# Kernel optimization log

Measured on AMD Instinct MI355X. Metric: run time of the kernel, lower is better.

The kernel has to match this reference:

```python
import jax, jax.numpy as jnp
import numpy as np

B, T, DM = 1, 8192, 1024
DS, DC, EXP = 16, 4, 2
DI = DM * EXP  # 2048


def setup_inputs() -> dict:
    key = jax.random.key(0)
    ks = jax.random.split(key, 6)
    sc = lambda k, shape, s: jax.random.normal(k, shape, jnp.float32) * s
    return {
        "x": jax.random.normal(ks[0], (B, T, DM), jnp.float32),
        "W_in": sc(ks[1], (DM, 2 * DI), 0.02),        # stored [in, out]
        "conv_w": sc(ks[2], (DI, 1, DC), 0.2),        # depthwise conv weight (OIH)
        "conv_b": jnp.zeros((DI,), jnp.float32),
        "W_x": sc(ks[3], (DI, 2 * DS + 1), 0.02),     # stored [in, out]
        "A_log": jnp.log(jnp.arange(1, DS + 1, dtype=jnp.float32)),
        "D": jnp.ones((DI,), jnp.float32),
        "W_out": sc(ks[4], (DI, DM), 0.02),           # stored [in, out]
    }


def reference(x, W_in, conv_w, conv_b, W_x, A_log, D, W_out):
    Bq, Tq, _ = x.shape
    # input projection and gate split
    xz = x @ W_in                              # [B,T,2*DI]
    xc, z = jnp.split(xz, 2, axis=-1)          # each [B,T,DI]
    # causal depthwise conv1d (pad left DC-1 == torch pad both + truncate [:T])
    xcT = jnp.transpose(xc, (0, 2, 1))         # [B,DI,T]
    conv = jax.lax.conv_general_dilated(
        xcT, conv_w, window_strides=(1,), padding=[(DC - 1, 0)],
        feature_group_count=DI)
    conv = conv + conv_b[None, :, None]
    xs = jax.nn.silu(jnp.transpose(conv, (0, 2, 1)))   # [B,T,DI]
    # selective SSM parameters (single shared delta per timestep)
    x_dbl = xs @ W_x                           # [B,T,2N+1]
    delta = jax.nn.softplus(x_dbl[..., :1])    # [B,T,1]
    Bp = x_dbl[..., 1:1 + DS]                  # [B,T,N]
    Cp = x_dbl[..., 1 + DS:]                   # [B,T,N]
    A = -jnp.exp(A_log)                        # [N]
    A_bar = jnp.exp(delta * A)                 # [B,T,N]
    B_bar = delta * Bp                         # [B,T,N]

    def step(h, inp):
        a_t, b_t, x_t, c_t = inp               # [B,N],[B,N],[B,DI],[B,N]
        h = a_t[:, None, :] * h + b_t[:, None, :] * x_t[:, :, None]  # [B,DI,N]
        y_t = jnp.einsum('bdn,bn->bd', h, c_t)
        return h, y_t

    h0 = jnp.zeros((Bq, DI, DS), xs.dtype)
    seq = (jnp.swapaxes(A_bar, 0, 1), jnp.swapaxes(B_bar, 0, 1),
           jnp.swapaxes(xs, 0, 1), jnp.swapaxes(Cp, 0, 1))
    _, ys = jax.lax.scan(step, h0, seq)        # ys: [T,B,DI]
    y = jnp.swapaxes(ys, 0, 1) + D * xs        # [B,T,DI]
    y = y * jax.nn.silu(z)
    return y @ W_out                           # [B,T,DM]
```

## Files before the change

kernel.cpp:

```cpp
#include <hip/hip_runtime.h>
#include <hip/hip_bf16.h>

#define T_SEQ 8192
#define DMODEL 1024
#define DINNER 2048
#define NSTATE 16
#define NCH 128
#define CL 64

typedef __attribute__((ext_vector_type(8))) short bf16x8;
typedef __attribute__((ext_vector_type(4))) float f32x4;

__device__ __forceinline__ float bf2f(ushort u) {
  union { unsigned u; float f; } c; c.u = ((unsigned)u) << 16; return c.f;
}
__device__ __forceinline__ ushort f2bf(float f) {
  union { float f; unsigned u; } c; c.f = f;
  unsigned r = c.u + 0x7FFFu + ((c.u >> 16) & 1u);
  return (ushort)(r >> 16);
}

#define GLD16(dst, src) __builtin_amdgcn_global_load_lds( \
    (const __attribute__((address_space(1))) void*)(src), \
    (__attribute__((address_space(3))) void*)(dst), 16, 0, 0)

template<int N> __device__ __forceinline__ void waitcnt_vm() {
  asm volatile("s_waitcnt vmcnt(%0)" :: "i"(N) : "memory");
}
#define LGKM0() do { asm volatile("s_waitcnt lgkmcnt(0)" ::: "memory"); \
                     __builtin_amdgcn_sched_barrier(0); } while (0)

__global__ __launch_bounds__(256) void cast_bf16(const float* __restrict__ in,
                                                 ushort* __restrict__ out, int n4) {
  int i = blockIdx.x * 256 + threadIdx.x;
  if (i < n4) {
    float4 v = ((const float4*)in)[i];
    ushort4 o;
    o.x = f2bf(v.x); o.y = f2bf(v.y); o.z = f2bf(v.z); o.w = f2bf(v.w);
    ((ushort4*)out)[i] = o;
  }
}

__global__ __launch_bounds__(256) void transpose_bf16(const float* __restrict__ in,
                                                      ushort* __restrict__ out, int R, int C) {
  __shared__ float tile[32][33];
  int bx = blockIdx.x * 32;
  int by = blockIdx.y * 32;
  int x = threadIdx.x, y = threadIdx.y;
#pragma unroll
  for (int j = 0; j < 32; j += 8)
    tile[y + j][x] = in[(size_t)(by + y + j) * C + bx + x];
  __syncthreads();
#pragma unroll
  for (int j = 0; j < 32; j += 8)
    out[(size_t)(bx + y + j) * R + by + x] = f2bf(tile[x][y + j]);
}

__global__ __launch_bounds__(256) void wx_transpose_pad(const float* __restrict__ Wx,
                                                        ushort* __restrict__ wxT) {
  int idx = blockIdx.x * 256 + threadIdx.x;
  int j = idx >> 11;
  int k = idx & 2047;
  wxT[idx] = (j < 33) ? f2bf(Wx[k * 33 + j]) : (ushort)0;
}

template<int OUTMODE>
__global__ __launch_bounds__(512, 2)
void gemm_pipe(const ushort* __restrict__ A, const ushort* __restrict__ B,
               void* __restrict__ out0, void* __restrict__ out1,
               int N, int K, int nbn) {
  extern __shared__ __align__(16) char smem[];
  char* const smemB = smem + 98304;

  const int tid = threadIdx.x, lane = tid & 63, wid = tid >> 6;
  const int wm = wid >> 1, wn = wid & 1;

  const int nwg = gridDim.x;
  const int q = nwg >> 3, r = nwg & 7;
  const int xcd = blockIdx.x & 7, bidx = blockIdx.x >> 3;
  const int wg = (xcd < r ? xcd * (q + 1) : r * (q + 1) + (xcd - r) * q) + bidx;
  const int mbase = (wg / nbn) * 256;
  const int nbase = (wg % nbn) * 128;
  const int NT = K >> 6;

  const int srow = tid >> 3;
  const int scb = ((tid & 7) << 4) ^ ((srow & 7) << 4);
  const ushort* pa[4];
  const ushort* pb[2];
#pragma unroll
  for (int j = 0; j < 4; ++j) pa[j] = A + (size_t)(mbase + j * 64 + srow) * K + (scb >> 1);
#pragma unroll
  for (int j = 0; j < 2; ++j) pb[j] = B + (size_t)(nbase + j * 64 + srow) * K + (scb >> 1);

#define STA(buf, j, tt) GLD16(smem  + (buf) * 32768 + (j) * 8192 + wid * 1024, pa[j] + (size_t)(tt) * 64)
#define STB(buf, j, tt) GLD16(smemB + (buf) * 16384 + (j) * 8192 + wid * 1024, pb[j] + (size_t)(tt) * 64)

  const int frow = lane & 15, hh = lane >> 4;
  const int cbk0 = (hh << 4) ^ ((frow & 7) << 4);
  const int cbk1 = (64 + (hh << 4)) ^ ((frow & 7) << 4);
  const int arow0 = (wm * 64 + frow) * 128;
  const int brow0 = (wn * 64 + frow) * 128;

  f32x4 acc[4][4];
#pragma unroll
  for (int m = 0; m < 4; ++m)
#pragma unroll
    for (int n = 0; n < 4; ++n) acc[m][n] = (f32x4){0.f, 0.f, 0.f, 0.f};

#pragma unroll
  for (int tt = 0; tt < 2; ++tt) {
    STA(tt, 0, tt); STA(tt, 1, tt); STA(tt, 2, tt); STA(tt, 3, tt);
    STB(tt, 0, tt); STB(tt, 1, tt);
  }
  waitcnt_vm<6>();
  __builtin_amdgcn_s_barrier();

  int cur = 0;
  for (int t = 0; t < NT; ++t) {
    const char* bA = smem + cur * 32768;
    const char* bB = smemB + cur * 16384;
    const int nxt = cur + 2 - ((cur >= 1) ? 3 : 0);
    const bool pf = (t + 2 < NT);
    bf16x8 alo[2][2], ahi[2][2], blo[2][2], bhi[2][2];

#pragma unroll
    for (int m = 0; m < 2; ++m) {
      alo[m][0] = *(const bf16x8*)(bA + arow0 + m * 2048 + cbk0);
      alo[m][1] = *(const bf16x8*)(bA + arow0 + m * 2048 + cbk1);
    }
#pragma unroll
    for (int n = 0; n < 2; ++n) {
      blo[n][0] = *(const bf16x8*)(bB + brow0 + n * 2048 + cbk0);
      blo[n][1] = *(const bf16x8*)(bB + brow0 + n * 2048 + cbk1);
    }
    if (pf) { STA(nxt, 0, t + 2); STA(nxt, 1, t + 2); }
    __builtin_amdgcn_s_barrier();
    LGKM0();
    __builtin_amdgcn_s_setprio(1);
#pragma unroll
    for (int m = 0; m < 2; ++m)
#pragma unroll
      for (int n = 0; n < 2; ++n)
#pragma unroll
        for (int kk = 0; kk < 2; ++kk)
          acc[m][n] = __builtin_amdgcn_mfma_f32_16x16x32_bf16(alo[m][kk], blo[n][kk], acc[m][n], 0, 0, 0);
    __builtin_amdgcn_s_setprio(0);
    __builtin_amdgcn_s_barrier();

#pragma unroll
    for (int m = 0; m < 2; ++m) {
      ahi[m][0] = *(const bf16x8*)(bA + arow0 + (2 + m) * 2048 + cbk0);
      ahi[m][1] = *(const bf16x8*)(bA + arow0 + (2 + m) * 2048 + cbk1);
    }
    if (pf) { STA(nxt, 2, t + 2); STA(nxt, 3, t + 2); }
    __builtin_amdgcn_s_barrier();
    LGKM0();
    __builtin_amdgcn_s_setprio(1);
#pragma unroll
    for (int m = 0; m < 2; ++m)
#pragma unroll
      for (int n = 0; n < 2; ++n)
#pragma unroll
        for (int kk = 0; kk < 2; ++kk)
          acc[2 + m][n] = __builtin_amdgcn_mfma_f32_16x16x32_bf16(ahi[m][kk], blo[n][kk], acc[2 + m][n], 0, 0, 0);
    __builtin_amdgcn_s_setprio(0);
    __builtin_amdgcn_s_barrier();

#pragma unroll
    for (int n = 0; n < 2; ++n) {
      bhi[n][0] = *(const bf16x8*)(bB + brow0 + (2 + n) * 2048 + cbk0);
      bhi[n][1] = *(const bf16x8*)(bB + brow0 + (2 + n) * 2048 + cbk1);
    }
    if (pf) STB(nxt, 0, t + 2);
    __builtin_amdgcn_s_barrier();
    LGKM0();
    __builtin_amdgcn_s_setprio(1);
#pragma unroll
    for (int m = 0; m < 2; ++m)
#pragma unroll
      for (int n = 0; n < 2; ++n)
#pragma unroll
        for (int kk = 0; kk < 2; ++kk)
          acc[2 + m][2 + n] = __builtin_amdgcn_mfma_f32_16x16x32_bf16(ahi[m][kk], bhi[n][kk], acc[2 + m][2 + n], 0, 0, 0);
    __builtin_amdgcn_s_setprio(0);
    __builtin_amdgcn_s_barrier();

    if (pf) STB(nxt, 1, t + 2);
    __builtin_amdgcn_s_setprio(1);
#pragma unroll
    for (int m = 0; m < 2; ++m)
#pragma unroll
      for (int n = 0; n < 2; ++n)
#pragma unroll
        for (int kk = 0; kk < 2; ++kk)
          acc[m][2 + n] = __builtin_amdgcn_mfma_f32_16x16x32_bf16(alo[m][kk], bhi[n][kk], acc[m][2 + n], 0, 0, 0);
    __builtin_amdgcn_s_setprio(0);
    if (pf) waitcnt_vm<6>(); else waitcnt_vm<0>();
    __builtin_amdgcn_s_barrier();

    cur = cur + 1 - ((cur == 2) ? 3 : 0);
  }

  const int crow0 = mbase + wm * 64 + (lane >> 4) * 4;
  const int ccol0 = nbase + wn * 64 + (lane & 15);
#pragma unroll
  for (int m = 0; m < 4; ++m)
#pragma unroll
    for (int n = 0; n < 4; ++n)
#pragma unroll
      for (int j = 0; j < 4; ++j) {
        int rr = crow0 + m * 16 + j;
        int cc = ccol0 + n * 16;
        float v = acc[m][n][j];
        if (OUTMODE == 0) {
          ((float*)out0)[(size_t)rr * N + cc] = v;
        } else {
          ushort* dst = (cc < 2048) ? (ushort*)out0 : (ushort*)out1;
          int c2 = cc & 2047;
          dst[(size_t)rr * 2048 + c2] = f2bf(v);
        }
      }
#undef STA
#undef STB
}

__global__ __launch_bounds__(256) void gemm_thin(const ushort* __restrict__ A,
                                                 const ushort* __restrict__ Bw,
                                                 float* __restrict__ part) {
  __shared__ __align__(16) ushort sA[128 * 64];
  __shared__ __align__(16) ushort sB[48 * 64];
  const int tid = threadIdx.x, lane = tid & 63, wid = tid >> 6;
  const int mbase = blockIdx.x * 128;
  const int kbase = blockIdx.y * 512;
  const int frow = lane & 15, fke = (lane >> 4) * 8;

  f32x4 acc[2][3];
#pragma unroll
  for (int m = 0; m < 2; ++m)
#pragma unroll
    for (int n = 0; n < 3; ++n) acc[m][n] = (f32x4){0.f, 0.f, 0.f, 0.f};

  for (int k0 = 0; k0 < 512; k0 += 64) {
#pragma unroll
    for (int j = 0; j < 4; ++j) {
      int o = tid * 16 + j * 4096;
      int row = o >> 7, ke = ((o >> 4) & 7) * 8;
      GLD16((char*)sA + wid * 1024 + j * 4096,
            A + (size_t)(mbase + row) * DINNER + kbase + k0 + ke);
    }
    for (int i = tid; i < 384; i += 256) {
      int brow = i >> 3, kc = (i & 7) * 8;
      *(bf16x8*)&sB[brow * 64 + kc] = *(const bf16x8*)(Bw + (size_t)brow * DINNER + kbase + k0 + kc);
    }
    __syncthreads();
    bf16x8 af[2][2], bf_[3][2];
#pragma unroll
    for (int m = 0; m < 2; ++m)
#pragma unroll
      for (int ks = 0; ks < 2; ++ks)
        af[m][ks] = *(const bf16x8*)&sA[(wid * 32 + m * 16 + frow) * 64 + ks * 32 + fke];
#pragma unroll
    for (int n = 0; n < 3; ++n)
#pragma unroll
      for (int ks = 0; ks < 2; ++ks)
        bf_[n][ks] = *(const bf16x8*)&sB[(n * 16 + frow) * 64 + ks * 32 + fke];
#pragma unroll
    for (int m = 0; m < 2; ++m)
#pragma unroll
      for (int n = 0; n < 3; ++n)
#pragma unroll
        for (int ks = 0; ks < 2; ++ks)
          acc[m][n] = __builtin_amdgcn_mfma_f32_16x16x32_bf16(af[m][ks], bf_[n][ks], acc[m][n], 0, 0, 0);
    __syncthreads();
  }
  float* po = part + (size_t)blockIdx.y * (T_SEQ * 48);
#pragma unroll
  for (int m = 0; m < 2; ++m)
#pragma unroll
    for (int n = 0; n < 3; ++n)
#pragma unroll
      for (int j = 0; j < 4; ++j) {
        int rr = mbase + wid * 32 + m * 16 + (lane >> 4) * 4 + j;
        int cc = n * 16 + (lane & 15);
        po[(size_t)rr * 48 + cc] = acc[m][n][j];
      }
}

__global__ __launch_bounds__(256) void reduce4(const float* __restrict__ part,
                                               float* __restrict__ xdbl) {
  int i = blockIdx.x * 256 + threadIdx.x;
  const float4* p = (const float4*)part;
  float4 a = p[i], b = p[i + 98304], c = p[i + 2 * 98304], d = p[i + 3 * 98304];
  ((float4*)xdbl)[i] = make_float4(a.x + b.x + c.x + d.x, a.y + b.y + c.y + d.y,
                                   a.z + b.z + c.z + d.z, a.w + b.w + c.w + d.w);
}

__global__ __launch_bounds__(256) void conv_silu(const ushort* __restrict__ xc,
                                                 const float* __restrict__ cw,
                                                 const float* __restrict__ cb,
                                                 ushort* __restrict__ xs) {
  int idx = blockIdx.x * 256 + threadIdx.x;
  int t = idx >> 11, d = idx & 2047;
  float4 w = *(const float4*)(cw + d * 4);
  float a = cb[d];
  const float wk[4] = {w.x, w.y, w.z, w.w};
#pragma unroll
  for (int k = 0; k < 4; ++k) {
    int tt = t - 3 + k;
    if (tt >= 0) a += bf2f(xc[(size_t)tt * 2048 + d]) * wk[k];
  }
  float s = a / (1.f + expf(-a));
  xs[idx] = f2bf(s);
}

__global__ __launch_bounds__(256) void precompute_k(const float* __restrict__ xdbl,
                                                    const float* __restrict__ A_log,
                                                    float* __restrict__ abar,
                                                    float* __restrict__ bbar,
                                                    float* __restrict__ cc,
                                                    float* __restrict__ dlt) {
  int t = blockIdx.x * 256 + threadIdx.x;
  if (t >= T_SEQ) return;
  const float* r = xdbl + (size_t)t * 48;
  float v = r[0];
  float delta = (v > 20.f) ? v : log1pf(expf(v));
  dlt[t] = delta;
#pragma unroll
  for (int n = 0; n < NSTATE; ++n) {
    float A = -expf(A_log[n]);
    abar[t * 16 + n] = expf(delta * A);
    bbar[t * 16 + n] = delta * r[1 + n];
    cc[t * 16 + n]   = r[17 + n];
  }
}

__global__ __launch_bounds__(256) void chunkprod_k(const float* __restrict__ dlt,
                                                   const float* __restrict__ A_log,
                                                   float* __restrict__ P) {
  int idx = blockIdx.x * 256 + threadIdx.x;
  if (idx >= NCH * NSTATE) return;
  int c = idx >> 4, n = idx & 15;
  float s = 0.f;
  for (int i = 0; i < CL; ++i) s += dlt[c * CL + i];
  P[idx] = expf(-expf(A_log[n]) * s);
}

__global__ __launch_bounds__(256) void scan1(const ushort* __restrict__ xs,
                                             const float* __restrict__ abar,
                                             const float* __restrict__ bbar,
                                             float* __restrict__ hend) {
  int c = blockIdx.x;
  int d = blockIdx.y * 256 + threadIdx.x;
  __shared__ float s_ab[CL * 16], s_bb[CL * 16];
  for (int e = threadIdx.x; e < CL * 16; e += 256) {
    s_ab[e] = abar[(size_t)c * CL * 16 + e];
    s_bb[e] = bbar[(size_t)c * CL * 16 + e];
  }
  __syncthreads();
  float h[16];
#pragma unroll
  for (int n = 0; n < 16; ++n) h[n] = 0.f;
  int tbase = c * CL;
  for (int i = 0; i < CL; ++i) {
    float x = bf2f(xs[(size_t)(tbase + i) * DINNER + d]);
#pragma unroll
    for (int n = 0; n < 16; ++n) h[n] = s_ab[i * 16 + n] * h[n] + s_bb[i * 16 + n] * x;
  }
  float* o = hend + ((size_t)c * DINNER + d) * 16;
#pragma unroll
  for (int qq = 0; qq < 4; ++qq)
    ((float4*)o)[qq] = make_float4(h[4 * qq], h[4 * qq + 1], h[4 * qq + 2], h[4 * qq + 3]);
}

__global__ __launch_bounds__(256) void scan2(const float* __restrict__ hend,
                                             const float* __restrict__ P,
                                             float* __restrict__ hin) {
  int idx = blockIdx.x * 256 + threadIdx.x;
  int n = idx & 15;
  float h = 0.f;
  for (int c = 0; c < NCH; ++c) {
    hin[(size_t)c * (DINNER * 16) + idx] = h;
    h = P[c * 16 + n] * h + hend[(size_t)c * (DINNER * 16) + idx];
  }
}

__global__ __launch_bounds__(256) void scan3(const ushort* __restrict__ xs,
                                             const ushort* __restrict__ zb,
                                             const float* __restrict__ abar,
                                             const float* __restrict__ bbar,
                                             const float* __restrict__ cc,
                                             const float* __restrict__ hin,
                                             const float* __restrict__ Dv,
                                             ushort* __restrict__ y) {
  int c = blockIdx.x;
  int d = blockIdx.y * 256 + threadIdx.x;
  __shared__ float s_ab[CL * 16], s_bb[CL * 16], s_cc[CL * 16];
  for (int e = threadIdx.x; e < CL * 16; e += 256) {
    s_ab[e] = abar[(size_t)c * CL * 16 + e];
    s_bb[e] = bbar[(size_t)c * CL * 16 + e];
    s_cc[e] = cc[(size_t)c * CL * 16 + e];
  }
  __syncthreads();
  float h[16];
  const float* hi = hin + ((size_t)c * DINNER + d) * 16;
#pragma unroll
  for (int qq = 0; qq < 4; ++qq) {
    float4 v = ((const float4*)hi)[qq];
    h[4 * qq] = v.x; h[4 * qq + 1] = v.y; h[4 * qq + 2] = v.z; h[4 * qq + 3] = v.w;
  }
  float Dd = Dv[d];
  int tbase = c * CL;
  for (int i = 0; i < CL; ++i) {
    size_t t = tbase + i;
    float x = bf2f(xs[t * DINNER + d]);
    float ys = 0.f;
#pragma unroll
    for (int n = 0; n < 16; ++n) {
      h[n] = s_ab[i * 16 + n] * h[n] + s_bb[i * 16 + n] * x;
      ys += s_cc[i * 16 + n] * h[n];
    }
    float z = bf2f(zb[t * 2048 + d]);
    float yv = (ys + Dd * x) * (z / (1.f + expf(-z)));
    y[t * DINNER + d] = f2bf(yv);
  }
}

extern "C" void kernel_launch(void* const* d_in, const int* in_sizes, int n_in,
                              void* d_out, int out_size, void* d_ws, size_t ws_size,
                              hipStream_t stream) {
  const float* x      = (const float*)d_in[0];
  const float* W_in   = (const float*)d_in[1];
  const float* conv_w = (const float*)d_in[2];
  const float* conv_b = (const float*)d_in[3];
  const float* W_x    = (const float*)d_in[4];
  const float* A_log  = (const float*)d_in[5];
  const float* Dv     = (const float*)d_in[6];
  const float* W_out  = (const float*)d_in[7];
  float* out = (float*)d_out;

  char* w = (char*)d_ws;
  auto alloc = [&](size_t bytes) { char* p = w; w += (bytes + 255) & ~(size_t)255; return p; };

  ushort* xbf   = (ushort*)alloc((size_t)T_SEQ * DMODEL * 2);
  ushort* winT  = (ushort*)alloc((size_t)4096 * 1024 * 2);
  ushort* woutT = (ushort*)alloc((size_t)1024 * 2048 * 2);
  ushort* wxT   = (ushort*)alloc((size_t)48 * 2048 * 2);
  ushort* xc    = (ushort*)alloc((size_t)T_SEQ * DINNER * 2);
  ushort* zb    = (ushort*)alloc((size_t)T_SEQ * DINNER * 2);
  ushort* xs    = (ushort*)alloc((size_t)T_SEQ * DINNER * 2);
  float*  xdbl  = (float*) alloc((size_t)T_SEQ * 48 * 4);
  float*  parts = (float*) alloc((size_t)4 * T_SEQ * 48 * 4);
  float*  abar  = (float*) alloc((size_t)T_SEQ * 16 * 4);
  float*  bbar  = (float*) alloc((size_t)T_SEQ * 16 * 4);
  float*  ccb   = (float*) alloc((size_t)T_SEQ * 16 * 4);
  float*  dlt   = (float*) alloc((size_t)T_SEQ * 4);
  float*  P     = (float*) alloc((size_t)NCH * 16 * 4);
  float*  hend  = (float*) alloc((size_t)NCH * DINNER * 16 * 4);
  float*  hin   = (float*) alloc((size_t)NCH * DINNER * 16 * 4);
  ushort* ybf   = (ushort*)alloc((size_t)T_SEQ * DINNER * 2);

  auto kg1 = gemm_pipe<1>;
  auto kg3 = gemm_pipe<0>;
  hipFuncSetAttribute(reinterpret_cast<const void*>(kg1),
                      hipFuncAttributeMaxDynamicSharedMemorySize, 147456);
  hipFuncSetAttribute(reinterpret_cast<const void*>(kg3),
                      hipFuncAttributeMaxDynamicSharedMemorySize, 147456);

  cast_bf16<<<(T_SEQ * DMODEL / 4 + 255) / 256, 256, 0, stream>>>(x, xbf, T_SEQ * DMODEL / 4);
  transpose_bf16<<<dim3(4096 / 32, 1024 / 32), dim3(32, 8), 0, stream>>>(W_in, winT, 1024, 4096);
  transpose_bf16<<<dim3(1024 / 32, 2048 / 32), dim3(32, 8), 0, stream>>>(W_out, woutT, 2048, 1024);
  wx_transpose_pad<<<(48 * 2048) / 256, 256, 0, stream>>>(W_x, wxT);

  kg1<<<dim3((T_SEQ / 256) * (4096 / 128)), 512, 147456, stream>>>(xbf, winT, xc, zb, 4096, 1024, 4096 / 128);

  conv_silu<<<(T_SEQ * DINNER) / 256, 256, 0, stream>>>(xc, conv_w, conv_b, xs);

  gemm_thin<<<dim3(T_SEQ / 128, 4), 256, 0, stream>>>(xs, wxT, parts);
  reduce4<<<(T_SEQ * 48 / 4) / 256, 256, 0, stream>>>(parts, xdbl);

  precompute_k<<<T_SEQ / 256, 256, 0, stream>>>(xdbl, A_log, abar, bbar, ccb, dlt);
  chunkprod_k<<<(NCH * 16 + 255) / 256, 256, 0, stream>>>(dlt, A_log, P);

  scan1<<<dim3(NCH, DINNER / 256), 256, 0, stream>>>(xs, abar, bbar, hend);
  scan2<<<(DINNER * 16) / 256, 256, 0, stream>>>(hend, P, hin);
  scan3<<<dim3(NCH, DINNER / 256), 256, 0, stream>>>(xs, zb, abar, bbar, ccb, hin, Dv, ybf);

  kg3<<<dim3((T_SEQ / 256) * (1024 / 128)), 512, 147456, stream>>>(ybf, woutT, out, nullptr, 1024, 2048, 1024 / 128);
}
```

Baseline: 316.8 us.

## Restructure GEMM to 128x256 tiles with 4 waves and K=32 steps; vectorize conv

New measurement: 375.1 us. 18.4% more time.

```diff
diff --git a/kernel.cpp b/kernel.cpp
--- a/kernel.cpp
+++ b/kernel.cpp
@@ -29,6 +29,8 @@
 }
 #define LGKM0() do { asm volatile("s_waitcnt lgkmcnt(0)" ::: "memory"); \
                      __builtin_amdgcn_sched_barrier(0); } while (0)
+#define BAR() do { __builtin_amdgcn_sched_barrier(0); __builtin_amdgcn_s_barrier(); \
+                   __builtin_amdgcn_sched_barrier(0); } while (0)
 
 __global__ __launch_bounds__(256) void cast_bf16(const float* __restrict__ in,
                                                  ushort* __restrict__ out, int n4) {
@@ -65,163 +67,132 @@
 }
 
 template<int OUTMODE>
-__global__ __launch_bounds__(512, 2)
+__global__ __launch_bounds__(256, 2)
 void gemm_pipe(const ushort* __restrict__ A, const ushort* __restrict__ B,
                void* __restrict__ out0, void* __restrict__ out1,
                int N, int K, int nbn) {
   extern __shared__ __align__(16) char smem[];
-  char* const smemB = smem + 98304;
+  char* const sBb = smem + 3 * 8192;
 
   const int tid = threadIdx.x, lane = tid & 63, wid = tid >> 6;
-  const int wm = wid >> 1, wn = wid & 1;
+  const int wn = wid;
 
   const int nwg = gridDim.x;
   const int q = nwg >> 3, r = nwg & 7;
   const int xcd = blockIdx.x & 7, bidx = blockIdx.x >> 3;
   const int wg = (xcd < r ? xcd * (q + 1) : r * (q + 1) + (xcd - r) * q) + bidx;
-  const int mbase = (wg / nbn) * 256;
-  const int nbase = (wg % nbn) * 128;
-  const int NT = K >> 6;
-
-  const int srow = tid >> 3;
-  const int scb = ((tid & 7) << 4) ^ ((srow & 7) << 4);
-  const ushort* pa[4];
-  const ushort* pb[2];
-#pragma unroll
-  for (int j = 0; j < 4; ++j) pa[j] = A + (size_t)(mbase + j * 64 + srow) * K + (scb >> 1);
-#pragma unroll
-  for (int j = 0; j < 2; ++j) pb[j] = B + (size_t)(nbase + j * 64 + srow) * K + (scb >> 1);
-
-#define STA(buf, j, tt) GLD16(smem  + (buf) * 32768 + (j) * 8192 + wid * 1024, pa[j] + (size_t)(tt) * 64)
-#define STB(buf, j, tt) GLD16(smemB + (buf) * 16384 + (j) * 8192 + wid * 1024, pb[j] + (size_t)(tt) * 64)
+  const int mbase = (wg / nbn) * 128;
+  const int nbase = (wg % nbn) * 256;
+  const int NT = K >> 5;
+
+  const ushort* pa[2];
+  const ushort* pb[4];
+#pragma unroll
+  for (int j = 0; j < 2; ++j) {
+    int idx = j * 256 + wid * 64 + lane;
+    int row = idx >> 2, g = idx & 3;
+    pa[j] = A + (size_t)(mbase + row) * K + (g ^ (row & 3)) * 8;
+  }
+#pragma unroll
+  for (int j = 0; j < 4; ++j) {
+    int idx = j * 256 + wid * 64 + lane;
+    int row = idx >> 2, g = idx & 3;
+    pb[j] = B + (size_t)(nbase + row) * K + (g ^ (row & 3)) * 8;
+  }
+
+#define STA(slot, tt) do { char* _d = smem + (slot) * 8192 + wid * 1024; \
+    GLD16(_d,        pa[0] + (size_t)(tt) * 32); \
+    GLD16(_d + 4096, pa[1] + (size_t)(tt) * 32); } while (0)
+#define STB01(slot, tt) do { char* _d = sBb + (slot) * 16384 + wid * 1024; \
+    GLD16(_d,        pb[0] + (size_t)(tt) * 32); \
+    GLD16(_d + 4096, pb[1] + (size_t)(tt) * 32); } while (0)
+#define STB23(slot, tt) do { char* _d = sBb + (slot) * 16384 + 8192 + wid * 1024; \
+    GLD16(_d,        pb[2] + (size_t)(tt) * 32); \
+    GLD16(_d + 4096, pb[3] + (size_t)(tt) * 32); } while (0)
 
   const int frow = lane & 15, hh = lane >> 4;
-  const int cbk0 = (hh << 4) ^ ((frow & 7) << 4);
-  const int cbk1 = (64 + (hh << 4)) ^ ((frow & 7) << 4);
-  const int arow0 = (wm * 64 + frow) * 128;
-  const int brow0 = (wn * 64 + frow) * 128;
-
-  f32x4 acc[4][4];
-#pragma unroll
-  for (int m = 0; m < 4; ++m)
+  const int gsw = (hh ^ (frow & 3)) << 4;
+  const int aoff = frow * 64 + gsw;
+  const int boff = (wn * 64 + frow) * 64 + gsw;
+
+  f32x4 acc[8][4];
+#pragma unroll
+  for (int m = 0; m < 8; ++m)
 #pragma unroll
     for (int n = 0; n < 4; ++n) acc[m][n] = (f32x4){0.f, 0.f, 0.f, 0.f};
 
-#pragma unroll
-  for (int tt = 0; tt < 2; ++tt) {
-    STA(tt, 0, tt); STA(tt, 1, tt); STA(tt, 2, tt); STA(tt, 3, tt);
-    STB(tt, 0, tt); STB(tt, 1, tt);
-  }
+  STA(0, 0); STB01(0, 0); STB23(0, 0);
+  STA(1, 1); STB01(1, 1); STB23(1, 1);
   waitcnt_vm<6>();
-  __builtin_amdgcn_s_barrier();
+  BAR();
 
   int cur = 0;
   for (int t = 0; t < NT; ++t) {
-    const char* bA = smem + cur * 32768;
-    const char* bB = smemB + cur * 16384;
+    const char* bA = smem + cur * 8192;
+    const char* bB = sBb + cur * 16384;
     const int nxt = cur + 2 - ((cur >= 1) ? 3 : 0);
     const bool pf = (t + 2 < NT);
-    bf16x8 alo[2][2], ahi[2][2], blo[2][2], bhi[2][2];
-
-#pragma unroll
-    for (int m = 0; m < 2; ++m) {
-      alo[m][0] = *(const bf16x8*)(bA + arow0 + m * 2048 + cbk0);
-      alo[m][1] = *(const bf16x8*)(bA + arow0 + m * 2048 + cbk1);
-    }
-#pragma unroll
-    for (int n = 0; n < 2; ++n) {
-      blo[n][0] = *(const bf16x8*)(bB + brow0 + n * 2048 + cbk0);
-      blo[n][1] = *(const bf16x8*)(bB + brow0 + n * 2048 + cbk1);
-    }
-    if (pf) { STA(nxt, 0, t + 2); STA(nxt, 1, t + 2); }
-    __builtin_amdgcn_s_barrier();
+    bf16x8 a[8], b0, b1, b2, b3;
+
+#pragma unroll
+    for (int m = 0; m < 8; ++m) a[m] = *(const bf16x8*)(bA + aoff + m * 1024);
+    b0 = *(const bf16x8*)(bB + boff);
+    b1 = *(const bf16x8*)(bB + boff + 1024);
+    if (pf) { STA(nxt, t + 2); STB01(nxt, t + 2); }
+    BAR();
     LGKM0();
     __builtin_amdgcn_s_setprio(1);
 #pragma unroll
-    for (int m = 0; m < 2; ++m)
-#pragma unroll
-      for (int n = 0; n < 2; ++n)
-#pragma unroll
-        for (int kk = 0; kk < 2; ++kk)
-          acc[m][n] = __builtin_amdgcn_mfma_f32_16x16x32_bf16(alo[m][kk], blo[n][kk], acc[m][n], 0, 0, 0);
+    for (int m = 0; m < 8; ++m) {
+      acc[m][0] = __builtin_amdgcn_mfma_f32_16x16x32_bf16(a[m], b0, acc[m][0], 0, 0, 0);
+      acc[m][1] = __builtin_amdgcn_mfma_f32_16x16x32_bf16(a[m], b1, acc[m][1], 0, 0, 0);
+    }
     __builtin_amdgcn_s_setprio(0);
-    __builtin_amdgcn_s_barrier();
-
-#pragma unroll
-    for (int m = 0; m < 2; ++m) {
-      ahi[m][0] = *(const bf16x8*)(bA + arow0 + (2 + m) * 2048 + cbk0);
-      ahi[m][1] = *(const bf16x8*)(bA + arow0 + (2 + m) * 2048 + cbk1);
-    }
-    if (pf) { STA(nxt, 2, t + 2); STA(nxt, 3, t + 2); }
-    __builtin_amdgcn_s_barrier();
+    BAR();
+
+    b2 = *(const bf16x8*)(bB + boff + 2048);
+    b3 = *(const bf16x8*)(bB + boff + 3072);
+    if (pf) STB23(nxt, t + 2);
+    BAR();
     LGKM0();
     __builtin_amdgcn_s_setprio(1);
 #pragma unroll
-    for (int m = 0; m < 2; ++m)
-#pragma unroll
-      for (int n = 0; n < 2; ++n)
-#pragma unroll
-        for (int kk = 0; kk < 2; ++kk)
-          acc[2 + m][n] = __builtin_amdgcn_mfma_f32_16x16x32_bf16(ahi[m][kk], blo[n][kk], acc[2 + m][n], 0, 0, 0);
-    __builtin_amdgcn_s_setprio(0);
-    __builtin_amdgcn_s_barrier();
-
-#pragma unroll
-    for (int n = 0; n < 2; ++n) {
-      bhi[n][0] = *(const bf16x8*)(bB + brow0 + (2 + n) * 2048 + cbk0);
-      bhi[n][1] = *(const bf16x8*)(bB + brow0 + (2 + n) * 2048 + cbk1);
-    }
-    if (pf) STB(nxt, 0, t + 2);
-    __builtin_amdgcn_s_barrier();
-    LGKM0();
-    __builtin_amdgcn_s_setprio(1);
-#pragma unroll
-    for (int m = 0; m < 2; ++m)
-#pragma unroll
-      for (int n = 0; n < 2; ++n)
-#pragma unroll
-        for (int kk = 0; kk < 2; ++kk)
-          acc[2 + m][2 + n] = __builtin_amdgcn_mfma_f32_16x16x32_bf16(ahi[m][kk], bhi[n][kk], acc[2 + m][2 + n], 0, 0, 0);
-    __builtin_amdgcn_s_setprio(0);
-    __builtin_amdgcn_s_barrier();
-
-    if (pf) STB(nxt, 1, t + 2);
-    __builtin_amdgcn_s_setprio(1);
-#pragma unroll
-    for (int m = 0; m < 2; ++m)
-#pragma unroll
-      for (int n = 0; n < 2; ++n)
-#pragma unroll
-        for (int kk = 0; kk < 2; ++kk)
-          acc[m][2 + n] = __builtin_amdgcn_mfma_f32_16x16x32_bf16(alo[m][kk], bhi[n][kk], acc[m][2 + n], 0, 0, 0);
+    for (int m = 0; m < 8; ++m) {
+      acc[m][2] = __builtin_amdgcn_mfma_f32_16x16x32_bf16(a[m], b2, acc[m][2], 0, 0, 0);
+      acc[m][3] = __builtin_amdgcn_mfma_f32_16x16x32_bf16(a[m], b3, acc[m][3], 0, 0, 0);
+    }
     __builtin_amdgcn_s_setprio(0);
     if (pf) waitcnt_vm<6>(); else waitcnt_vm<0>();
-    __builtin_amdgcn_s_barrier();
+    BAR();
 
     cur = cur + 1 - ((cur == 2) ? 3 : 0);
   }
 
-  const int crow0 = mbase + wm * 64 + (lane >> 4) * 4;
-  const int ccol0 = nbase + wn * 64 + (lane & 15);
-#pragma unroll
-  for (int m = 0; m < 4; ++m)
-#pragma unroll
-    for (int n = 0; n < 4; ++n)
-#pragma unroll
-      for (int j = 0; j < 4; ++j) {
-        int rr = crow0 + m * 16 + j;
-        int cc = ccol0 + n * 16;
-        float v = acc[m][n][j];
-        if (OUTMODE == 0) {
-          ((float*)out0)[(size_t)rr * N + cc] = v;
-        } else {
-          ushort* dst = (cc < 2048) ? (ushort*)out0 : (ushort*)out1;
-          int c2 = cc & 2047;
-          dst[(size_t)rr * 2048 + c2] = f2bf(v);
-        }
-      }
+  const int crow0 = mbase + (lane >> 4) * 4;
+  const int ccol0 = wn * 64 + (lane & 15);
+  if (OUTMODE == 0) {
+    float* po = (float*)out0;
+#pragma unroll
+    for (int m = 0; m < 8; ++m)
+#pragma unroll
+      for (int n = 0; n < 4; ++n)
+#pragma unroll
+        for (int j = 0; j < 4; ++j)
+          po[(size_t)(crow0 + m * 16 + j) * N + nbase + ccol0 + n * 16] = acc[m][n][j];
+  } else {
+    ushort* dst = (nbase < 2048) ? (ushort*)out0 : (ushort*)out1;
+    const int cb = (nbase & 2047) + ccol0;
+#pragma unroll
+    for (int m = 0; m < 8; ++m)
+#pragma unroll
+      for (int n = 0; n < 4; ++n)
+#pragma unroll
+        for (int j = 0; j < 4; ++j)
+          dst[(size_t)(crow0 + m * 16 + j) * 2048 + cb + n * 16] = f2bf(acc[m][n][j]);
+  }
 #undef STA
-#undef STB
+#undef STB01
+#undef STB23
 }
 
 __global__ __launch_bounds__(256) void gemm_thin(const ushort* __restrict__ A,
@@ -300,17 +271,26 @@
                                                  const float* __restrict__ cb,
                                                  ushort* __restrict__ xs) {
   int idx = blockIdx.x * 256 + threadIdx.x;
-  int t = idx >> 11, d = idx & 2047;
-  float4 w = *(const float4*)(cw + d * 4);
-  float a = cb[d];
-  const float wk[4] = {w.x, w.y, w.z, w.w};
+  int t = idx >> 8, d0 = (idx & 255) << 3;
+  float a[8];
+#pragma unroll
+  for (int e = 0; e < 8; ++e) a[e] = cb[d0 + e];
 #pragma unroll
   for (int k = 0; k < 4; ++k) {
     int tt = t - 3 + k;
-    if (tt >= 0) a += bf2f(xc[(size_t)tt * 2048 + d]) * wk[k];
-  }
-  float s = a / (1.f + expf(-a));
-  xs[idx] = f2bf(s);
+    if (tt >= 0) {
+      bf16x8 v = *(const bf16x8*)(xc + (size_t)tt * 2048 + d0);
+#pragma unroll
+      for (int e = 0; e < 8; ++e) a[e] += bf2f((ushort)v[e]) * cw[(d0 + e) * 4 + k];
+    }
+  }
+  bf16x8 o;
+#pragma unroll
+  for (int e = 0; e < 8; ++e) {
+    float s = a[e] / (1.f + expf(-a[e]));
+    o[e] = (short)f2bf(s);
+  }
+  *(bf16x8*)(xs + (size_t)t * 2048 + d0) = o;
 }
 
 __global__ __launch_bounds__(256) void precompute_k(const float* __restrict__ xdbl,
@@ -462,18 +442,18 @@
   auto kg1 = gemm_pipe<1>;
   auto kg3 = gemm_pipe<0>;
   hipFuncSetAttribute(reinterpret_cast<const void*>(kg1),
-                      hipFuncAttributeMaxDynamicSharedMemorySize, 147456);
+                      hipFuncAttributeMaxDynamicSharedMemorySize, 73728);
   hipFuncSetAttribute(reinterpret_cast<const void*>(kg3),
-                      hipFuncAttributeMaxDynamicSharedMemorySize, 147456);
+                      hipFuncAttributeMaxDynamicSharedMemorySize, 73728);
 
   cast_bf16<<<(T_SEQ * DMODEL / 4 + 255) / 256, 256, 0, stream>>>(x, xbf, T_SEQ * DMODEL / 4);
   transpose_bf16<<<dim3(4096 / 32, 1024 / 32), dim3(32, 8), 0, stream>>>(W_in, winT, 1024, 4096);
   transpose_bf16<<<dim3(1024 / 32, 2048 / 32), dim3(32, 8), 0, stream>>>(W_out, woutT, 2048, 1024);
   wx_transpose_pad<<<(48 * 2048) / 256, 256, 0, stream>>>(W_x, wxT);
 
-  kg1<<<dim3((T_SEQ / 256) * (4096 / 128)), 512, 147456, stream>>>(xbf, winT, xc, zb, 4096, 1024, 4096 / 128);
-
-  conv_silu<<<(T_SEQ * DINNER) / 256, 256, 0, stream>>>(xc, conv_w, conv_b, xs);
+  kg1<<<dim3((T_SEQ / 128) * (4096 / 256)), 256, 73728, stream>>>(xbf, winT, xc, zb, 4096, 1024, 4096 / 256);
+
+  conv_silu<<<(T_SEQ * 256) / 256, 256, 0, stream>>>(xc, conv_w, conv_b, xs);
 
   gemm_thin<<<dim3(T_SEQ / 128, 4), 256, 0, stream>>>(xs, wxT, parts);
   reduce4<<<(T_SEQ * 48 / 4) / 256, 256, 0, stream>>>(parts, xdbl);
@@ -485,5 +465,5 @@
   scan2<<<(DINNER * 16) / 256, 256, 0, stream>>>(hend, P, hin);
   scan3<<<dim3(NCH, DINNER / 256), 256, 0, stream>>>(xs, zb, abar, bbar, ccb, hin, Dv, ybf);
 
-  kg3<<<dim3((T_SEQ / 256) * (1024 / 128)), 512, 147456, stream>>>(ybf, woutT, out, nullptr, 1024, 2048, 1024 / 128);
-}
+  kg3<<<dim3((T_SEQ / 128) * (1024 / 256)), 256, 73728, stream>>>(ybf, woutT, out, nullptr, 1024, 2048, 1024 / 256);
+}
```
